# Kernel tuning notes

Hardware: AMD Instinct MI355X
Metric: run time of the kernel (lower is better)

The kernel has to match this reference:

```python
import jax, jax.numpy as jnp
import numpy as np

UP = 2                # upsample_factor
FILTER_SIZE = 31      # sinc filter kernel size (odd)
CUTOFF = 0.5 / UP     # cutoff frequency (fraction of Nyquist)
LEAKY_SLOPE = 0.01    # torch F.leaky_relu default


def make_sinc_filter(cutoff_freq, filter_size):
    # matches torch: t = linspace(-filter_size//2, filter_size//2, filter_size)
    lo = (-filter_size) // 2  # Python floor division: -31//2 = -16
    hi = filter_size // 2     # 15
    t = jnp.linspace(float(lo), float(hi), filter_size)
    x, y = jnp.meshgrid(t, t, indexing='ij')
    r = jnp.sqrt(x ** 2 + y ** 2) + 1e-10
    f = jnp.sin(2.0 * np.pi * cutoff_freq * r) / (np.pi * r)
    return f / jnp.sum(f)


def _ac_coords(out_n, in_n, dtype):
    # align_corners=True mapping: src = i * (in_n - 1) / (out_n - 1)
    scale = (in_n - 1) / (out_n - 1)
    c = jnp.arange(out_n, dtype=dtype) * jnp.asarray(scale, dtype)
    i0 = jnp.clip(jnp.floor(c).astype(jnp.int32), 0, in_n - 2)
    w = c - i0.astype(dtype)
    return i0, w


def bilinear_ac(x, out_h, out_w):
    # x: [B, C, H, W] -> [B, C, out_h, out_w], bilinear, align_corners=True
    H, W = x.shape[-2], x.shape[-1]
    i0, wy = _ac_coords(out_h, H, x.dtype)
    j0, wx = _ac_coords(out_w, W, x.dtype)
    # rows
    top = x[:, :, i0, :]
    bot = x[:, :, i0 + 1, :]
    xr = top + (bot - top) * wy[:, None]          # [B, C, out_h, W]
    # cols
    left = xr[:, :, :, j0]
    right = xr[:, :, :, j0 + 1]
    return left + (right - left) * wx             # [B, C, out_h, out_w]


def setup_inputs() -> dict:
    key = jax.random.key(0)
    x = jax.random.normal(key, (8, 64, 128, 128), dtype=jnp.float32)
    filt = make_sinc_filter(CUTOFF, FILTER_SIZE).astype(jnp.float32)  # buffer, deterministic
    return {"x": x, "filt": filt}


def reference(x, filt):
    B, C, H, W = x.shape
    k = filt.shape[0]
    up = bilinear_ac(x, H * UP, W * UP)
    # 2) elementwise activation
    act = jax.nn.leaky_relu(up, LEAKY_SLOPE)
    # 3) depthwise sinc low-pass conv, same padding
    kernel = jnp.broadcast_to(filt[None, None], (C, 1, k, k))  # [C,1,k,k]
    filtered = jax.lax.conv_general_dilated(
        act, kernel,
        window_strides=(1, 1),
        padding=[(k // 2, k // 2), (k // 2, k // 2)],
        feature_group_count=C,
        dimension_numbers=('NCHW', 'OIHW', 'NCHW'),
    )
    # 4) bilinear downsample back to original size (align_corners=True)
    return bilinear_ac(filtered, H, W)
```

## Files before the change

### kernel.cpp

```cpp
#include <hip/hip_runtime.h>
#include <hip/hip_bf16.h>

typedef __attribute__((ext_vector_type(8))) short bf16x8;
typedef __attribute__((ext_vector_type(16))) float f32x16;

#define INH   128
#define LEAK  0.01f
#define USTR  120
#define UROWS 158
#define GSTR  288

__device__ __forceinline__ unsigned short f2bf(float f) {
    __hip_bfloat16 h = __float2bfloat16(f);
    return *(unsigned short*)&h;
}

__device__ __forceinline__ float upsample_one(const float* __restrict__ xc,
                                              int ur, int uc, float UPS) {
    float cr = (float)ur * UPS;
    int r0 = (int)cr; if (r0 > 126) r0 = 126;
    float wr = cr - (float)r0;
    float cs = (float)uc * UPS;
    int s0 = (int)cs; if (s0 > 126) s0 = 126;
    float ws = cs - (float)s0;
    const float* p = xc + r0 * INH + s0;
    float a = p[0], b = p[1], c = p[INH], d = p[INH + 1];
    float top = a + (c - a) * wr;
    float bot = b + (d - b) * wr;
    float val = top + (bot - top) * ws;
    return (val > 0.0f) ? val : (LEAK * val);
}

__global__ void build_table(const float* __restrict__ filt, unsigned short* __restrict__ tab) {
    int idx = blockIdx.x * 256 + threadIdx.x;
    if (idx >= 31 * 4 * 64) return;
    int lane = idx & 63, c = (idx >> 6) & 3, fr = idx >> 8;
    #pragma unroll
    for (int t = 0; t < 8; ++t) {
        int v = 16 * c + 8 * (lane >> 5) + t - (lane & 31);
        float f = (v >= 0 && v <= 30) ? filt[fr * 31 + v] : 0.0f;
        tab[idx * 8 + t] = f2bf(f);
    }
}

__global__ __launch_bounds__(256)
void upsample_act(const float* __restrict__ x, unsigned short* __restrict__ U) {
    const float UPS = (float)(127.0 / 255.0);
    int idx = blockIdx.x * 256 + threadIdx.x;
    int bc = idx / (256 * 72);
    int rem = idx - bc * (256 * 72);
    int r = rem / 72;
    int c4 = (rem - r * 72) * 4;
    const float* __restrict__ xc = x + (size_t)bc * (INH * INH);
    unsigned short o[4];
    #pragma unroll
    for (int e = 0; e < 4; ++e) {
        int uc = c4 + e - 15;
        float val = 0.0f;
        if ((unsigned)uc < 256u) val = upsample_one(xc, r, uc, UPS);
        o[e] = f2bf(val);
    }
    *(uint2*)&U[((size_t)bc * 256 + r) * GSTR + c4] = *(const uint2*)o;
}

__global__ __launch_bounds__(256)
void conv_ds(const unsigned short* __restrict__ U, const unsigned short* __restrict__ tab,
             float* __restrict__ out) {
    __shared__ unsigned short T[UROWS * USTR];
    const int tid = threadIdx.x;
    const int bx = blockIdx.x;
    const int by = blockIdx.y;
    const int bc = blockIdx.z;
    const float DNS = (float)(255.0 / 127.0);
    const int pr0 = 128 * by, pc0 = 64 * bx;
    const unsigned short* __restrict__ Ub = U + (size_t)bc * 256 * GSTR;

    #pragma unroll
    for (int k = 0; k < 8; ++k) {
        int c = tid + k * 256;
        if (c < UROWS * 12) {
            int row = c / 12;
            int sub = c - row * 12;
            int gr = pr0 + row - 15;
            uint4 v = {0u, 0u, 0u, 0u};
            if ((unsigned)gr < 256u)
                v = *(const uint4*)(Ub + gr * GSTR + pc0 + sub * 8);
            *(uint4*)&T[row * USTR + sub * 8] = v;
        }
    }
    __syncthreads();

    const int lane = tid & 63;
    const int w = tid >> 6;
    const int wxs = w & 1, wys = w >> 1;
    const int r32 = lane & 31;
    const int hk = lane >> 5;

    const char* ub = (const char*)T + (64 * wys + r32) * (USTR * 2) + (32 * wxs + 8 * hk) * 2;
    const bf16x8* tv = (const bf16x8*)tab;

    f32x16 acc0 = {0.f,0.f,0.f,0.f,0.f,0.f,0.f,0.f,0.f,0.f,0.f,0.f,0.f,0.f,0.f,0.f};
    f32x16 acc1 = acc0;

    #pragma unroll 1
    for (int fr = 0; fr < 31; ++fr) {
        bf16x8 B0 = tv[(fr * 4 + 0) * 64 + lane];
        bf16x8 B1 = tv[(fr * 4 + 1) * 64 + lane];
        bf16x8 B2 = tv[(fr * 4 + 2) * 64 + lane];
        bf16x8 B3 = tv[(fr * 4 + 3) * 64 + lane];
        const char* u0 = ub + fr * (USTR * 2);
        const char* u1 = u0 + 32 * (USTR * 2);
        bf16x8 a;
        a = *(const bf16x8*)(u0 + 0);
        acc0 = __builtin_amdgcn_mfma_f32_32x32x16_bf16(a, B0, acc0, 0, 0, 0);
        a = *(const bf16x8*)(u0 + 32);
        acc0 = __builtin_amdgcn_mfma_f32_32x32x16_bf16(a, B1, acc0, 0, 0, 0);
        a = *(const bf16x8*)(u0 + 64);
        acc0 = __builtin_amdgcn_mfma_f32_32x32x16_bf16(a, B2, acc0, 0, 0, 0);
        a = *(const bf16x8*)(u0 + 96);
        acc0 = __builtin_amdgcn_mfma_f32_32x32x16_bf16(a, B3, acc0, 0, 0, 0);
        a = *(const bf16x8*)(u1 + 0);
        acc1 = __builtin_amdgcn_mfma_f32_32x32x16_bf16(a, B0, acc1, 0, 0, 0);
        a = *(const bf16x8*)(u1 + 32);
        acc1 = __builtin_amdgcn_mfma_f32_32x32x16_bf16(a, B1, acc1, 0, 0, 0);
        a = *(const bf16x8*)(u1 + 64);
        acc1 = __builtin_amdgcn_mfma_f32_32x32x16_bf16(a, B2, acc1, 0, 0, 0);
        a = *(const bf16x8*)(u1 + 96);
        acc1 = __builtin_amdgcn_mfma_f32_32x32x16_bf16(a, B3, acc1, 0, 0, 0);
    }

    const int cc = 64 * bx + 32 * wxs + r32;
    const bool doout = (cc & 1) == 0;
    const int oj = cc >> 1;
    const float wxw = (float)oj * DNS - (float)cc;

    #pragma unroll
    for (int tt = 0; tt < 2; ++tt) {
        int cr0 = 128 * by + 64 * wys + 32 * tt;
        #pragma unroll
        for (int p = 0; p < 8; ++p) {
            int rpe = ((p & 1) << 1) + ((p >> 1) << 3) + 4 * hk;
            int cre = cr0 + rpe;
            int oi = cre >> 1;
            float wyw = (float)oi * DNS - (float)cre;
            float ae, ao;
            if (tt == 0) { ae = acc0[2 * p]; ao = acc0[2 * p + 1]; }
            else         { ae = acc1[2 * p]; ao = acc1[2 * p + 1]; }
            float v = ae + (ao - ae) * wyw;
            float vr = __shfl_xor(v, 1, 64);
            if (doout) {
                float o = v + (vr - v) * wxw;
                out[((size_t)bc * 128 + oi) * 128 + oj] = o;
            }
        }
    }
}

__global__ __launch_bounds__(256)
void afa_mfma(const float* __restrict__ x, const unsigned short* __restrict__ tab,
              float* __restrict__ out) {
    __shared__ unsigned short Ut[UROWS * USTR];
    const int tid = threadIdx.x;
    const int bx = blockIdx.x, by = blockIdx.y, bc = blockIdx.z;
    const float* __restrict__ xc = x + (size_t)bc * (INH * INH);
    const float UPS = (float)(127.0 / 255.0);
    const float DNS = (float)(255.0 / 127.0);
    const int pr0 = 128 * by, pc0 = 64 * bx;

    for (int idx = tid; idx < UROWS * (USTR / 2); idx += 256) {
        int lr = idx / (USTR / 2);
        int lc0 = (idx - lr * (USTR / 2)) * 2;
        unsigned pack = 0;
        #pragma unroll
        for (int e = 0; e < 2; ++e) {
            int lc = lc0 + e;
            int ur = pr0 + lr - 15;
            int uc = pc0 + lc - 15;
            float val = 0.0f;
            if (lc < 96 && (unsigned)ur < 256u && (unsigned)uc < 256u)
                val = upsample_one(xc, ur, uc, UPS);
            pack |= (unsigned)f2bf(val) << (16 * e);
        }
        *(unsigned*)&Ut[lr * USTR + lc0] = pack;
    }
    __syncthreads();

    const int lane = tid & 63;
    const int w = tid >> 6;
    const int wxs = w & 1, wys = w >> 1;
    const int r32 = lane & 31;
    const int hk = lane >> 5;
    const char* ub = (const char*)Ut + (64 * wys + r32) * (USTR * 2) + (32 * wxs + 8 * hk) * 2;
    const bf16x8* tv = (const bf16x8*)tab;
    f32x16 acc0 = {0.f,0.f,0.f,0.f,0.f,0.f,0.f,0.f,0.f,0.f,0.f,0.f,0.f,0.f,0.f,0.f};
    f32x16 acc1 = acc0;

    #pragma unroll 1
    for (int fr = 0; fr < 31; ++fr) {
        bf16x8 B0 = tv[(fr * 4 + 0) * 64 + lane];
        bf16x8 B1 = tv[(fr * 4 + 1) * 64 + lane];
        bf16x8 B2 = tv[(fr * 4 + 2) * 64 + lane];
        bf16x8 B3 = tv[(fr * 4 + 3) * 64 + lane];
        const char* u0 = ub + fr * (USTR * 2);
        const char* u1 = u0 + 32 * (USTR * 2);
        bf16x8 a;
        a = *(const bf16x8*)(u0 + 0);
        acc0 = __builtin_amdgcn_mfma_f32_32x32x16_bf16(a, B0, acc0, 0, 0, 0);
        a = *(const bf16x8*)(u0 + 32);
        acc0 = __builtin_amdgcn_mfma_f32_32x32x16_bf16(a, B1, acc0, 0, 0, 0);
        a = *(const bf16x8*)(u0 + 64);
        acc0 = __builtin_amdgcn_mfma_f32_32x32x16_bf16(a, B2, acc0, 0, 0, 0);
        a = *(const bf16x8*)(u0 + 96);
        acc0 = __builtin_amdgcn_mfma_f32_32x32x16_bf16(a, B3, acc0, 0, 0, 0);
        a = *(const bf16x8*)(u1 + 0);
        acc1 = __builtin_amdgcn_mfma_f32_32x32x16_bf16(a, B0, acc1, 0, 0, 0);
        a = *(const bf16x8*)(u1 + 32);
        acc1 = __builtin_amdgcn_mfma_f32_32x32x16_bf16(a, B1, acc1, 0, 0, 0);
        a = *(const bf16x8*)(u1 + 64);
        acc1 = __builtin_amdgcn_mfma_f32_32x32x16_bf16(a, B2, acc1, 0, 0, 0);
        a = *(const bf16x8*)(u1 + 96);
        acc1 = __builtin_amdgcn_mfma_f32_32x32x16_bf16(a, B3, acc1, 0, 0, 0);
    }

    const int cc = 64 * bx + 32 * wxs + r32;
    const bool doout = (cc & 1) == 0;
    const int oj = cc >> 1;
    const float wxw = (float)oj * DNS - (float)cc;
    #pragma unroll
    for (int tt = 0; tt < 2; ++tt) {
        int cr0 = 128 * by + 64 * wys + 32 * tt;
        #pragma unroll
        for (int p = 0; p < 8; ++p) {
            int rpe = ((p & 1) << 1) + ((p >> 1) << 3) + 4 * hk;
            int cre = cr0 + rpe;
            int oi = cre >> 1;
            float wyw = (float)oi * DNS - (float)cre;
            float ae, ao;
            if (tt == 0) { ae = acc0[2 * p]; ao = acc0[2 * p + 1]; }
            else         { ae = acc1[2 * p]; ao = acc1[2 * p + 1]; }
            float v = ae + (ao - ae) * wyw;
            float vr = __shfl_xor(v, 1, 64);
            if (doout) {
                float o = v + (vr - v) * wxw;
                out[((size_t)bc * 128 + oi) * 128 + oj] = o;
            }
        }
    }
}

extern "C" void kernel_launch(void* const* d_in, const int* in_sizes, int n_in,
                              void* d_out, int out_size, void* d_ws, size_t ws_size,
                              hipStream_t stream) {
    const float* x    = (const float*)d_in[0];
    const float* filt = (const float*)d_in[1];
    float* out = (float*)d_out;

    unsigned short* tab = (unsigned short*)d_ws;
    const size_t U_OFF  = 131072;
    const size_t U_NEED = U_OFF + (size_t)512 * 256 * GSTR * 2;

    build_table<<<31, 256, 0, stream>>>(filt, tab);

    if (ws_size >= U_NEED) {
        unsigned short* U = (unsigned short*)((char*)d_ws + U_OFF);
        upsample_act<<<512 * 256 * 72 / 256, 256, 0, stream>>>(x, U);
        dim3 grid(4, 2, 8 * 64);
        conv_ds<<<grid, dim3(256), 0, stream>>>(U, tab, out);
    } else {
        dim3 grid(4, 2, 8 * 64);
        afa_mfma<<<grid, dim3(256), 0, stream>>>(x, tab, out);
    }
}
```

Before: 174.6 us.

## Retile conv to wide 64x128 tiles with shared A-fragment reuse and merged table launch

The conv tile shape changes from 128x64 to 64x128 output pixels, so the LDS halo shrinks (94x168 instead of 158x120), and each wave now computes two column-adjacent 32x32 blocks. Those blocks share overlapping A fragments, so six LDS loads feed eight MFMAs per filter row instead of eight. The filter-table build is folded into the upsample kernel as extra blocks to remove one launch, and launch bounds plus an unroll of 2 are added to raise occupancy and ILP. The risk is higher register pressure from holding six A fragments, and a wider LDS row stride that may introduce bank conflicts.

```diff
diff --git a/kernel.cpp b/kernel.cpp
--- a/kernel.cpp
+++ b/kernel.cpp
@@ -6,9 +6,9 @@
 
 #define INH   128
 #define LEAK  0.01f
-#define USTR  120
-#define UROWS 158
 #define GSTR  288
+#define TSTR  168
+#define TROWS 94
 
 __device__ __forceinline__ unsigned short f2bf(float f) {
     __hip_bfloat16 h = __float2bfloat16(f);
@@ -44,9 +44,23 @@
 }
 
 __global__ __launch_bounds__(256)
-void upsample_act(const float* __restrict__ x, unsigned short* __restrict__ U) {
+void up_table(const float* __restrict__ x, const float* __restrict__ filt,
+              unsigned short* __restrict__ U, unsigned short* __restrict__ tab) {
+    const int tid = threadIdx.x;
+    if (blockIdx.x < 31) {
+        int idx = blockIdx.x * 256 + tid;
+        if (idx >= 31 * 4 * 64) return;
+        int lane = idx & 63, c = (idx >> 6) & 3, fr = idx >> 8;
+        #pragma unroll
+        for (int t = 0; t < 8; ++t) {
+            int v = 16 * c + 8 * (lane >> 5) + t - (lane & 31);
+            float f = (v >= 0 && v <= 30) ? filt[fr * 31 + v] : 0.0f;
+            tab[idx * 8 + t] = f2bf(f);
+        }
+        return;
+    }
     const float UPS = (float)(127.0 / 255.0);
-    int idx = blockIdx.x * 256 + threadIdx.x;
+    int idx = (blockIdx.x - 31) * 256 + tid;
     int bc = idx / (256 * 72);
     int rem = idx - bc * (256 * 72);
     int r = rem / 72;
@@ -63,30 +77,122 @@
     *(uint2*)&U[((size_t)bc * 256 + r) * GSTR + c4] = *(const uint2*)o;
 }
 
-__global__ __launch_bounds__(256)
+__global__ __launch_bounds__(256, 4)
 void conv_ds(const unsigned short* __restrict__ U, const unsigned short* __restrict__ tab,
              float* __restrict__ out) {
-    __shared__ unsigned short T[UROWS * USTR];
+    __shared__ unsigned short T[TROWS * TSTR];
     const int tid = threadIdx.x;
     const int bx = blockIdx.x;
     const int by = blockIdx.y;
     const int bc = blockIdx.z;
     const float DNS = (float)(255.0 / 127.0);
-    const int pr0 = 128 * by, pc0 = 64 * bx;
-    const unsigned short* __restrict__ Ub = U + (size_t)bc * 256 * GSTR;
+    const int pr0 = 64 * by;
+    const unsigned short* __restrict__ Ub = U + (size_t)bc * 256 * GSTR + bx * 128;
 
     #pragma unroll
     for (int k = 0; k < 8; ++k) {
         int c = tid + k * 256;
-        if (c < UROWS * 12) {
-            int row = c / 12;
-            int sub = c - row * 12;
+        if (c < TROWS * 20) {
+            int row = c / 20;
+            int sub = c - row * 20;
             int gr = pr0 + row - 15;
             uint4 v = {0u, 0u, 0u, 0u};
             if ((unsigned)gr < 256u)
-                v = *(const uint4*)(Ub + gr * GSTR + pc0 + sub * 8);
-            *(uint4*)&T[row * USTR + sub * 8] = v;
-        }
+                v = *(const uint4*)(Ub + gr * GSTR + sub * 8);
+            *(uint4*)&T[row * TSTR + sub * 8] = v;
+        }
+    }
+    __syncthreads();
+
+    const int lane = tid & 63;
+    const int w = tid >> 6;
+    const int wxs = w & 1;
+    const int band = w >> 1;
+    const int r32 = lane & 31;
+    const int hk = lane >> 5;
+
+    const char* ab = (const char*)T + (32 * band + r32) * (TSTR * 2) + (64 * wxs + 8 * hk) * 2;
+    const bf16x8* tv = (const bf16x8*)tab;
+
+    f32x16 acc0 = {0.f,0.f,0.f,0.f,0.f,0.f,0.f,0.f,0.f,0.f,0.f,0.f,0.f,0.f,0.f,0.f};
+    f32x16 acc1 = acc0;
+
+    #pragma unroll 2
+    for (int fr = 0; fr < 31; ++fr) {
+        bf16x8 B0 = tv[(fr * 4 + 0) * 64 + lane];
+        bf16x8 B1 = tv[(fr * 4 + 1) * 64 + lane];
+        bf16x8 B2 = tv[(fr * 4 + 2) * 64 + lane];
+        bf16x8 B3 = tv[(fr * 4 + 3) * 64 + lane];
+        const char* u = ab + fr * (TSTR * 2);
+        bf16x8 A0 = *(const bf16x8*)(u + 0);
+        bf16x8 A1 = *(const bf16x8*)(u + 32);
+        bf16x8 A2 = *(const bf16x8*)(u + 64);
+        bf16x8 A3 = *(const bf16x8*)(u + 96);
+        bf16x8 A4 = *(const bf16x8*)(u + 128);
+        bf16x8 A5 = *(const bf16x8*)(u + 160);
+        acc0 = __builtin_amdgcn_mfma_f32_32x32x16_bf16(A0, B0, acc0, 0, 0, 0);
+        acc1 = __builtin_amdgcn_mfma_f32_32x32x16_bf16(A2, B0, acc1, 0, 0, 0);
+        acc0 = __builtin_amdgcn_mfma_f32_32x32x16_bf16(A1, B1, acc0, 0, 0, 0);
+        acc1 = __builtin_amdgcn_mfma_f32_32x32x16_bf16(A3, B1, acc1, 0, 0, 0);
+        acc0 = __builtin_amdgcn_mfma_f32_32x32x16_bf16(A2, B2, acc0, 0, 0, 0);
+        acc1 = __builtin_amdgcn_mfma_f32_32x32x16_bf16(A4, B2, acc1, 0, 0, 0);
+        acc0 = __builtin_amdgcn_mfma_f32_32x32x16_bf16(A3, B3, acc0, 0, 0, 0);
+        acc1 = __builtin_amdgcn_mfma_f32_32x32x16_bf16(A5, B3, acc1, 0, 0, 0);
+    }
+
+    #pragma unroll
+    for (int s = 0; s < 2; ++s) {
+        int cc = 128 * bx + 64 * wxs + 32 * s + r32;
+        const bool doout = (cc & 1) == 0;
+        const int oj = cc >> 1;
+        const float wxw = (float)oj * DNS - (float)cc;
+        #pragma unroll
+        for (int p = 0; p < 8; ++p) {
+            int rpe = ((p & 1) << 1) + ((p >> 1) << 3) + 4 * hk;
+            int cre = 64 * by + 32 * band + rpe;
+            int oi = cre >> 1;
+            float wyw = (float)oi * DNS - (float)cre;
+            float ae, ao;
+            if (s == 0) { ae = acc0[2 * p]; ao = acc0[2 * p + 1]; }
+            else        { ae = acc1[2 * p]; ao = acc1[2 * p + 1]; }
+            float v = ae + (ao - ae) * wyw;
+            float vr = __shfl_xor(v, 1, 64);
+            if (doout) {
+                float o = v + (vr - v) * wxw;
+                out[((size_t)bc * 128 + oi) * 128 + oj] = o;
+            }
+        }
+    }
+}
+
+#define FUSTR  120
+#define FUROWS 158
+__global__ __launch_bounds__(256)
+void afa_mfma(const float* __restrict__ x, const unsigned short* __restrict__ tab,
+              float* __restrict__ out) {
+    __shared__ unsigned short Ut[FUROWS * FUSTR];
+    const int tid = threadIdx.x;
+    const int bx = blockIdx.x, by = blockIdx.y, bc = blockIdx.z;
+    const float* __restrict__ xc = x + (size_t)bc * (INH * INH);
+    const float UPS = (float)(127.0 / 255.0);
+    const float DNS = (float)(255.0 / 127.0);
+    const int pr0 = 128 * by, pc0 = 64 * bx;
+
+    for (int idx = tid; idx < FUROWS * (FUSTR / 2); idx += 256) {
+        int lr = idx / (FUSTR / 2);
+        int lc0 = (idx - lr * (FUSTR / 2)) * 2;
+        unsigned pack = 0;
+        #pragma unroll
+        for (int e = 0; e < 2; ++e) {
+            int lc = lc0 + e;
+            int ur = pr0 + lr - 15;
+            int uc = pc0 + lc - 15;
+            float val = 0.0f;
+            if (lc < 96 && (unsigned)ur < 256u && (unsigned)uc < 256u)
+                val = upsample_one(xc, ur, uc, UPS);
+            pack |= (unsigned)f2bf(val) << (16 * e);
+        }
+        *(unsigned*)&Ut[lr * FUSTR + lc0] = pack;
     }
     __syncthreads();
 
@@ -95,10 +201,8 @@
     const int wxs = w & 1, wys = w >> 1;
     const int r32 = lane & 31;
     const int hk = lane >> 5;
-
-    const char* ub = (const char*)T + (64 * wys + r32) * (USTR * 2) + (32 * wxs + 8 * hk) * 2;
+    const char* ub = (const char*)Ut + (64 * wys + r32) * (FUSTR * 2) + (32 * wxs + 8 * hk) * 2;
     const bf16x8* tv = (const bf16x8*)tab;
-
     f32x16 acc0 = {0.f,0.f,0.f,0.f,0.f,0.f,0.f,0.f,0.f,0.f,0.f,0.f,0.f,0.f,0.f,0.f};
     f32x16 acc1 = acc0;
 
@@ -108,8 +212,8 @@
         bf16x8 B1 = tv[(fr * 4 + 1) * 64 + lane];
         bf16x8 B2 = tv[(fr * 4 + 2) * 64 + lane];
         bf16x8 B3 = tv[(fr * 4 + 3) * 64 + lane];
-        const char* u0 = ub + fr * (USTR * 2);
-        const char* u1 = u0 + 32 * (USTR * 2);
+        const char* u0 = ub + fr * (FUSTR * 2);
+        const char* u1 = u0 + 32 * (FUSTR * 2);
         bf16x8 a;
         a = *(const bf16x8*)(u0 + 0);
         acc0 = __builtin_amdgcn_mfma_f32_32x32x16_bf16(a, B0, acc0, 0, 0, 0);
@@ -133,7 +237,6 @@
     const bool doout = (cc & 1) == 0;
     const int oj = cc >> 1;
     const float wxw = (float)oj * DNS - (float)cc;
-
     #pragma unroll
     for (int tt = 0; tt < 2; ++tt) {
         int cr0 = 128 * by + 64 * wys + 32 * tt;
@@ -156,98 +259,6 @@
     }
 }
 
-__global__ __launch_bounds__(256)
-void afa_mfma(const float* __restrict__ x, const unsigned short* __restrict__ tab,
-              float* __restrict__ out) {
-    __shared__ unsigned short Ut[UROWS * USTR];
-    const int tid = threadIdx.x;
-    const int bx = blockIdx.x, by = blockIdx.y, bc = blockIdx.z;
-    const float* __restrict__ xc = x + (size_t)bc * (INH * INH);
-    const float UPS = (float)(127.0 / 255.0);
-    const float DNS = (float)(255.0 / 127.0);
-    const int pr0 = 128 * by, pc0 = 64 * bx;
-
-    for (int idx = tid; idx < UROWS * (USTR / 2); idx += 256) {
-        int lr = idx / (USTR / 2);
-        int lc0 = (idx - lr * (USTR / 2)) * 2;
-        unsigned pack = 0;
-        #pragma unroll
-        for (int e = 0; e < 2; ++e) {
-            int lc = lc0 + e;
-            int ur = pr0 + lr - 15;
-            int uc = pc0 + lc - 15;
-            float val = 0.0f;
-            if (lc < 96 && (unsigned)ur < 256u && (unsigned)uc < 256u)
-                val = upsample_one(xc, ur, uc, UPS);
-            pack |= (unsigned)f2bf(val) << (16 * e);
-        }
-        *(unsigned*)&Ut[lr * USTR + lc0] = pack;
-    }
-    __syncthreads();
-
-    const int lane = tid & 63;
-    const int w = tid >> 6;
-    const int wxs = w & 1, wys = w >> 1;
-    const int r32 = lane & 31;
-    const int hk = lane >> 5;
-    const char* ub = (const char*)Ut + (64 * wys + r32) * (USTR * 2) + (32 * wxs + 8 * hk) * 2;
-    const bf16x8* tv = (const bf16x8*)tab;
-    f32x16 acc0 = {0.f,0.f,0.f,0.f,0.f,0.f,0.f,0.f,0.f,0.f,0.f,0.f,0.f,0.f,0.f,0.f};
-    f32x16 acc1 = acc0;
-
-    #pragma unroll 1
-    for (int fr = 0; fr < 31; ++fr) {
-        bf16x8 B0 = tv[(fr * 4 + 0) * 64 + lane];
-        bf16x8 B1 = tv[(fr * 4 + 1) * 64 + lane];
-        bf16x8 B2 = tv[(fr * 4 + 2) * 64 + lane];
-        bf16x8 B3 = tv[(fr * 4 + 3) * 64 + lane];
-        const char* u0 = ub + fr * (USTR * 2);
-        const char* u1 = u0 + 32 * (USTR * 2);
-        bf16x8 a;
-        a = *(const bf16x8*)(u0 + 0);
-        acc0 = __builtin_amdgcn_mfma_f32_32x32x16_bf16(a, B0, acc0, 0, 0, 0);
-        a = *(const bf16x8*)(u0 + 32);
-        acc0 = __builtin_amdgcn_mfma_f32_32x32x16_bf16(a, B1, acc0, 0, 0, 0);
-        a = *(const bf16x8*)(u0 + 64);
-        acc0 = __builtin_amdgcn_mfma_f32_32x32x16_bf16(a, B2, acc0, 0, 0, 0);
-        a = *(const bf16x8*)(u0 + 96);
-        acc0 = __builtin_amdgcn_mfma_f32_32x32x16_bf16(a, B3, acc0, 0, 0, 0);
-        a = *(const bf16x8*)(u1 + 0);
-        acc1 = __builtin_amdgcn_mfma_f32_32x32x16_bf16(a, B0, acc1, 0, 0, 0);
-        a = *(const bf16x8*)(u1 + 32);
-        acc1 = __builtin_amdgcn_mfma_f32_32x32x16_bf16(a, B1, acc1, 0, 0, 0);
-        a = *(const bf16x8*)(u1 + 64);
-        acc1 = __builtin_amdgcn_mfma_f32_32x32x16_bf16(a, B2, acc1, 0, 0, 0);
-        a = *(const bf16x8*)(u1 + 96);
-        acc1 = __builtin_amdgcn_mfma_f32_32x32x16_bf16(a, B3, acc1, 0, 0, 0);
-    }
-
-    const int cc = 64 * bx + 32 * wxs + r32;
-    const bool doout = (cc & 1) == 0;
-    const int oj = cc >> 1;
-    const float wxw = (float)oj * DNS - (float)cc;
-    #pragma unroll
-    for (int tt = 0; tt < 2; ++tt) {
-        int cr0 = 128 * by + 64 * wys + 32 * tt;
-        #pragma unroll
-        for (int p = 0; p < 8; ++p) {
-            int rpe = ((p & 1) << 1) + ((p >> 1) << 3) + 4 * hk;
-            int cre = cr0 + rpe;
-            int oi = cre >> 1;
-            float wyw = (float)oi * DNS - (float)cre;
-            float ae, ao;
-            if (tt == 0) { ae = acc0[2 * p]; ao = acc0[2 * p + 1]; }
-            else         { ae = acc1[2 * p]; ao = acc1[2 * p + 1]; }
-            float v = ae + (ao - ae) * wyw;
-            float vr = __shfl_xor(v, 1, 64);
-            if (doout) {
-                float o = v + (vr - v) * wxw;
-                out[((size_t)bc * 128 + oi) * 128 + oj] = o;
-            }
-        }
-    }
-}
-
 extern "C" void kernel_launch(void* const* d_in, const int* in_sizes, int n_in,
                               void* d_out, int out_size, void* d_ws, size_t ws_size,
                               hipStream_t stream) {
@@ -259,14 +270,13 @@
     const size_t U_OFF  = 131072;
     const size_t U_NEED = U_OFF + (size_t)512 * 256 * GSTR * 2;
 
-    build_table<<<31, 256, 0, stream>>>(filt, tab);
-
     if (ws_size >= U_NEED) {
         unsigned short* U = (unsigned short*)((char*)d_ws + U_OFF);
-        upsample_act<<<512 * 256 * 72 / 256, 256, 0, stream>>>(x, U);
-        dim3 grid(4, 2, 8 * 64);
+        up_table<<<31 + 512 * 256 * 72 / 256, 256, 0, stream>>>(x, filt, U, tab);
+        dim3 grid(2, 4, 8 * 64);
         conv_ds<<<grid, dim3(256), 0, stream>>>(U, tab, out);
     } else {
+        build_table<<<31, 256, 0, stream>>>(filt, tab);
         dim3 grid(4, 2, 8 * 64);
         afa_mfma<<<grid, dim3(256), 0, stream>>>(x, tab, out);
     }
```

Result: faster. 165.6 us (-5.2%).
